# Performance work log

Hardware: AMD Instinct MI355X
Metric: run time of the kernel (lower is better)

Reference implementation:

```python
import jax, jax.numpy as jnp
import numpy as np

S = 192          # spatial_size
N = 100000       # active input sites
CIN, M, M2, NCLS = 3, 32, 64, 50
EPS = 1e-4       # scn BatchNorm eps
OFFS = np.array([[dx, dy, dz] for dx in (-1, 0, 1) for dy in (-1, 0, 1) for dz in (-1, 0, 1)], dtype=np.int64)


def _build_nbr(coords, size):
    # coords: [n,3] unique int64. Returns [n,27] int32 neighbor index (-1 = inactive site),
    # i.e. the submanifold-convolution rulebook built via sorted-key hashing.
    n = coords.shape[0]
    keys = (coords[:, 0] * size + coords[:, 1]) * size + coords[:, 2]
    order = np.argsort(keys)
    sk = keys[order]
    nbr = np.full((n, 27), -1, dtype=np.int32)
    for k, off in enumerate(OFFS):
        nc = coords + off
        ok = np.all((nc >= 0) & (nc < size), axis=1)
        qk = (nc[:, 0] * size + nc[:, 1]) * size + nc[:, 2]
        pos = np.searchsorted(sk, qk).clip(0, n - 1)
        hit = ok & (sk[pos] == qk)
        nbr[hit, k] = order[pos[hit]].astype(np.int32)
    return nbr


def setup_inputs() -> dict:
    rng = np.random.default_rng(0)
    raw = rng.integers(0, S, size=(130000, 3), dtype=np.int64)
    keys = (raw[:, 0] * S + raw[:, 1]) * S + raw[:, 2]
    _, first = np.unique(keys, return_index=True)
    coords = raw[np.sort(first)][:N]          # N unique active voxels
    nbr_fine = _build_nbr(coords, S)
    # stride-2 / filter-2 downsample rulebook: coarse sites = unique(coords // 2)
    S2 = S // 2
    cc = coords // 2
    ckeys = (cc[:, 0] * S2 + cc[:, 1]) * S2 + cc[:, 2]
    uk, parent = np.unique(ckeys, return_inverse=True)
    ccoords = np.column_stack((uk // (S2 * S2), (uk // S2) % S2, uk % S2))
    nbr_coarse = _build_nbr(ccoords, S2)
    offset_id = (coords[:, 0] % 2) * 4 + (coords[:, 1] % 2) * 2 + coords[:, 2] % 2
    key = jax.random.key(0)
    ks = jax.random.split(key, 8)
    def w(k, shape, fan):
        return jax.random.normal(k, shape, jnp.float32) * (1.0 / np.sqrt(fan))
    return dict(
        coords=jnp.asarray(coords, jnp.int32),
        features=jax.random.normal(ks[0], (N, CIN), jnp.float32),
        nbr_fine=jnp.asarray(nbr_fine),
        nbr_coarse=jnp.asarray(nbr_coarse),
        parent=jnp.asarray(parent.astype(np.int32)),
        offset_id=jnp.asarray(offset_id.astype(np.int32)),
        num_coarse=int(uk.shape[0]),
        w_in=w(ks[1], (27, CIN, M), 27 * CIN),
        w_b1=w(ks[2], (27, M, M), 27 * M),
        w_down=w(ks[3], (8, M, M2), 8 * M),
        w_b2=w(ks[4], (27, M2, M2), 27 * M2),
        w_up=w(ks[5], (8, M2, M), 8 * M2),
        w_b3=w(ks[6], (27, 2 * M, M), 27 * 2 * M),
        g1=jnp.ones((M,)), b1=jnp.zeros((M,)),
        gd=jnp.ones((M,)), bd=jnp.zeros((M,)),
        g2=jnp.ones((M2,)), b2=jnp.zeros((M2,)),
        gu=jnp.ones((M2,)), bu=jnp.zeros((M2,)),
        g3=jnp.ones((2 * M,)), b3=jnp.zeros((2 * M,)),
        go=jnp.ones((M,)), bo=jnp.zeros((M,)),
        w_lin=w(ks[7], (M, NCLS), M),
        b_lin=jnp.zeros((NCLS,)),
    )


def _subm_conv(f, nbr, W):
    # f: [n,Cin], nbr: [n,27] (-1 = inactive), W: [27,Cin,Cout]
    mask = nbr >= 0
    g = f[jnp.where(mask, nbr, 0)] * mask[..., None]  # [n,27,Cin]
    return jnp.einsum('nkc,kcd->nd', g, W)


def _bnrelu(f, gamma, beta):
    mu = f.mean(0)
    var = ((f - mu) ** 2).mean(0)
    return jax.nn.relu((f - mu) * (gamma / jnp.sqrt(var + EPS)) + beta)


def _down(f, parent, off_id, W, nc):
    # strided 2^3 conv: out[parent] += W[offset(child)] @ f[child]
    out = jnp.zeros((nc, W.shape[2]), f.dtype)
    for o in range(8):
        sel = (off_id == o)[:, None].astype(f.dtype)
        out = out + jax.ops.segment_sum((f * sel) @ W[o], parent, num_segments=nc)
    return out


def _up(g, parent, off_id, W):
    # 2^3 deconv back to fine sites
    gp = g[parent]
    out = jnp.zeros((gp.shape[0], W.shape[2]), g.dtype)
    for o in range(8):
        out = out + (off_id == o)[:, None].astype(g.dtype) * (gp @ W[o])
    return out


def reference(coords, features, nbr_fine, nbr_coarse, parent, offset_id, num_coarse,
              w_in, w_b1, w_down, w_b2, w_up, w_b3,
              g1, b1, gd, bd, g2, b2, gu, bu, g3, b3, go, bo, w_lin, b_lin):
    # InputLayer (coords unique -> identity) + SubmanifoldConvolution(CIN->M)
    f = _subm_conv(features, nbr_fine, w_in)
    # UNet level 0 block (pre-activation)
    f = _subm_conv(_bnrelu(f, g1, b1), nbr_fine, w_b1)
    skip = f
    # downsample: BNReLU + Convolution(M->M2, 2, 2)
    g = _down(_bnrelu(f, gd, bd), parent, offset_id, w_down, num_coarse)
    # UNet level 1 block
    g = _subm_conv(_bnrelu(g, g2, b2), nbr_coarse, w_b2)
    # upsample: BNReLU + Deconvolution(M2->M, 2, 2)
    u = _up(_bnrelu(g, gu, bu), parent, offset_id, w_up)
    # JoinTable + block (2M -> M)
    f = jnp.concatenate([skip, u], axis=1)
    f = _subm_conv(_bnrelu(f, g3, b3), nbr_fine, w_b3)
    # top-level BatchNormReLU(M) + OutputLayer + Linear head
    f = _bnrelu(f, go, bo)
    return f @ w_lin + b_lin
```

## Files before the change

kernel.cpp:

```cpp
#include <hip/hip_runtime.h>

#define EPS_BN 1e-4f
constexpr int BLK = 256;
constexpr int ECAPC = 1856;
constexpr int NCOPY = 8;

__global__ __launch_bounds__(64) void build_fine_k(
    const int* __restrict__ nbr, int n, int* __restrict__ cnt, int* __restrict__ ent) {
  int i = blockIdx.x * 64 + threadIdx.x;
  if (i >= n) return;
  int c = 0;
  const int* nr = nbr + (size_t)i * 27;
  int* er = ent + (size_t)i * 27;
#pragma unroll 1
  for (int k = 0; k < 27; ++k) {
    int j = nr[k];
    if (j >= 0) er[c++] = (k << 18) | j;
  }
  cnt[i] = c;
}

__global__ __launch_bounds__(64) void build_subm4_k(
    const int* __restrict__ nbr, int n,
    int* __restrict__ segP, int* __restrict__ ent) {
  int T = blockIdx.x, r = threadIdx.x;
  int i = T * 64 + r;
  bool valid = i < n;
  int base = 0;
#pragma unroll 1
  for (int k = 0; k < 27; ++k) {
    int j = valid ? nbr[(size_t)i * 27 + k] : -1;
    bool act = j >= 0;
    unsigned long long mb = __ballot(act);
    int cnt = __popcll(mb);
    int pre = __popcll(mb & ((1ull << r) - 1));
    if (act) ent[(size_t)T * ECAPC + base + pre] = (r << 23) | (k << 18) | j;
    int padded = (cnt + 3) & ~3;
    if (r < padded - cnt) ent[(size_t)T * ECAPC + base + cnt + r] = -1;
    base += padded;
  }
  if (r == 0) segP[T] = base;
}

__global__ __launch_bounds__(BLK) void child_scatter_k(
    const int* __restrict__ parent, const int* __restrict__ offid, int n,
    int* __restrict__ ccnt, int* __restrict__ cent) {
  int i = blockIdx.x * BLK + threadIdx.x;
  if (i >= n) return;
  int p = parent[i];
  int slot = atomicAdd(&ccnt[p], 1);
  cent[p * 8 + slot] = i | (offid[i] << 25);
}

template <int CI, int CO, int MODE>
__global__ __launch_bounds__(BLK) void tconvA_k(
    const float* __restrict__ in, const int* __restrict__ ent, const int* __restrict__ cnt,
    const int* __restrict__ parent, const int* __restrict__ offid,
    const float* __restrict__ W, float* __restrict__ out, int n,
    float* __restrict__ osums) {
  constexpr int LANES = CO / 4, SLOTS = BLK / LANES, RPS = 64 / SLOTS;
  __shared__ float red[2 * CO];
  int t = threadIdx.x;
  for (int idx = t; idx < 2 * CO; idx += BLK) red[idx] = 0.f;
  __syncthreads();
  int slot = t / LANES, lane = t % LANES, g = lane * 4;
  int T = blockIdx.x;
  float ssum[4] = {0, 0, 0, 0}, ssq[4] = {0, 0, 0, 0};
#pragma unroll 1
  for (int rr = 0; rr < RPS; ++rr) {
    int row = T * 64 + slot * RPS + rr;
    bool vrow = row < n;
    float a0 = 0.f, a1 = 0.f, a2 = 0.f, a3 = 0.f;
    int ec = 0;
    if (vrow) ec = (MODE == 2) ? 1 : cnt[row];
#pragma unroll 1
    for (int e = 0; e < ec; ++e) {
      int k, j;
      if constexpr (MODE == 0) {
        int v = ent[(size_t)row * 27 + e];
        k = (v >> 18) & 31; j = v & 0x3FFFF;
      } else if constexpr (MODE == 1) {
        int v = ent[(size_t)row * 8 + e];
        k = v >> 25; j = v & 0x1FFFFFF;
      } else {
        k = offid[row]; j = parent[row];
      }
      const float* Wk = W + (size_t)k * (CI * CO) + g;
      const float* xr = in + (size_t)j * CI;
#pragma unroll
      for (int h = 0; h < CI / 32; ++h) {
        float4 xv[8];
#pragma unroll
        for (int c4 = 0; c4 < 8; ++c4)
          xv[c4] = *reinterpret_cast<const float4*>(xr + h * 32 + c4 * 4);
#pragma unroll
        for (int c4 = 0; c4 < 8; ++c4) {
          float xs[4] = {xv[c4].x, xv[c4].y, xv[c4].z, xv[c4].w};
#pragma unroll
          for (int q = 0; q < 4; ++q) {
            float4 wv = *reinterpret_cast<const float4*>(Wk + (size_t)(h * 32 + c4 * 4 + q) * CO);
            a0 = fmaf(xs[q], wv.x, a0);
            a1 = fmaf(xs[q], wv.y, a1);
            a2 = fmaf(xs[q], wv.z, a2);
            a3 = fmaf(xs[q], wv.w, a3);
          }
        }
      }
    }
    if (vrow)
      *reinterpret_cast<float4*>(out + (size_t)row * CO + g) = make_float4(a0, a1, a2, a3);
    ssum[0] += a0; ssum[1] += a1; ssum[2] += a2; ssum[3] += a3;
    ssq[0] = fmaf(a0, a0, ssq[0]); ssq[1] = fmaf(a1, a1, ssq[1]);
    ssq[2] = fmaf(a2, a2, ssq[2]); ssq[3] = fmaf(a3, a3, ssq[3]);
  }
#pragma unroll
  for (int q = 0; q < 4; ++q) {
    atomicAdd(&red[g + q], ssum[q]);
    atomicAdd(&red[CO + g + q], ssq[q]);
  }
  __syncthreads();
  int copy = blockIdx.x & (NCOPY - 1);
  if (t < 2 * CO) atomicAdd(&osums[copy * 2 * CO + t], red[t]);
}

template <int CI, int CO>
__global__ __launch_bounds__(BLK) void tconvB_k(
    const float* __restrict__ in, const int* __restrict__ segP,
    const int* __restrict__ ent, int ecap,
    const float* __restrict__ W, float* __restrict__ out, int n,
    float* __restrict__ osums) {
  constexpr int GO = CO / 16;
  constexpr int AP = CO + 4;
  __shared__ float lacc[64 * AP];
  int t = threadIdx.x, T = blockIdx.x;
  for (int idx = t; idx < 64 * AP; idx += BLK) lacc[idx] = 0.f;
  __syncthreads();
  int P = segP[T];
  const int* entT = ent + (size_t)T * ecap;
  int slot = t >> 4, g = (t & 15) * GO;
#pragma unroll 1
  for (int pb = slot * 4; pb < P; pb += 64) {
    int ee[4] = {entT[pb], entT[pb + 1], entT[pb + 2], entT[pb + 3]};
    int k = (ee[0] >> 18) & 31;
    const float* Wk = W + (size_t)k * (CI * CO);
    float acc[4][GO];
#pragma unroll
    for (int pp = 0; pp < 4; ++pp)
#pragma unroll
      for (int b = 0; b < GO; ++b) acc[pp][b] = 0.f;
#pragma unroll 4
    for (int c4 = 0; c4 < CI / 4; ++c4) {
      int cb = c4 * 4;
      float xs[4][4];
#pragma unroll
      for (int pp = 0; pp < 4; ++pp) {
        float4 x = make_float4(0.f, 0.f, 0.f, 0.f);
        if (ee[pp] >= 0) {
          int j = ee[pp] & 0x3FFFF;
          x = *reinterpret_cast<const float4*>(in + (size_t)j * CI + cb);
        }
        xs[pp][0] = x.x; xs[pp][1] = x.y; xs[pp][2] = x.z; xs[pp][3] = x.w;
      }
#pragma unroll
      for (int q = 0; q < 4; ++q) {
        float4 w4 = *reinterpret_cast<const float4*>(Wk + (size_t)(cb + q) * CO + g);
        float wv[4] = {w4.x, w4.y, w4.z, w4.w};
#pragma unroll
        for (int pp = 0; pp < 4; ++pp)
#pragma unroll
          for (int b = 0; b < GO; ++b)
            acc[pp][b] = fmaf(xs[pp][q], wv[b], acc[pp][b]);
      }
    }
#pragma unroll
    for (int pp = 0; pp < 4; ++pp) {
      if (ee[pp] >= 0) {
        int r = (ee[pp] >> 23) & 63;
        float* ap = &lacc[r * AP + g];
#pragma unroll
        for (int b = 0; b < GO; ++b) atomicAdd(ap + b, acc[pp][b]);
      }
    }
  }
  __syncthreads();
  for (int idx = t; idx < 64 * (CO / 4); idx += BLK) {
    int r = idx / (CO / 4), c4 = idx - r * (CO / 4);
    int row = T * 64 + r;
    if (row < n)
      *reinterpret_cast<float4*>(out + (size_t)row * CO + c4 * 4) =
          *reinterpret_cast<const float4*>(&lacc[r * AP + c4 * 4]);
  }
  int copy = blockIdx.x & (NCOPY - 1);
  if (t < CO) {
    float s = 0.f, ss = 0.f;
#pragma unroll 4
    for (int r = 0; r < 64; ++r) {
      float x = lacc[r * AP + t];
      s += x; ss = fmaf(x, x, ss);
    }
    atomicAdd(&osums[copy * 2 * CO + t], s);
    atomicAdd(&osums[copy * 2 * CO + CO + t], ss);
  }
}

template <int C>
__global__ __launch_bounds__(BLK) void bnact_k(
    const float* __restrict__ in, const float* __restrict__ sums,
    const float* __restrict__ gm, const float* __restrict__ bt, float invn,
    float* __restrict__ outp, int n) {
  __shared__ float lst[2 * C];
  int t = threadIdx.x;
  if (t < C) {
    float s = 0.f, q = 0.f;
#pragma unroll
    for (int cp = 0; cp < NCOPY; ++cp) { s += sums[cp * 2 * C + t]; q += sums[cp * 2 * C + C + t]; }
    float mu = s * invn, var = q * invn - mu * mu;
    float sc = gm[t] / sqrtf(var + EPS_BN);
    lst[t] = sc; lst[C + t] = bt[t] - mu * sc;
  }
  __syncthreads();
  int total = n * (C / 4);
  const float4* in4 = reinterpret_cast<const float4*>(in);
  float4* out4 = reinterpret_cast<float4*>(outp);
  for (int idx = blockIdx.x * BLK + t; idx < total; idx += gridDim.x * BLK) {
    int cb = (idx & (C / 4 - 1)) * 4;
    float4 x = in4[idx];
    float v[4] = {x.x, x.y, x.z, x.w};
#pragma unroll
    for (int q = 0; q < 4; ++q) {
      float y = fmaf(v[q], lst[cb + q], lst[C + cb + q]);
      v[q] = y > 0.f ? y : 0.f;
    }
    out4[idx] = make_float4(v[0], v[1], v[2], v[3]);
  }
}

__global__ __launch_bounds__(BLK) void bncat_k(
    const float* __restrict__ fa, const float* __restrict__ sA,
    const float* __restrict__ gA, const float* __restrict__ bA,
    const float* __restrict__ fb, const float* __restrict__ sB,
    const float* __restrict__ gB, const float* __restrict__ bB,
    float invn, float* __restrict__ acat, int n) {
  __shared__ float lst[128];
  int t = threadIdx.x;
  if (t < 64) {
    int half = t >> 5, c = t & 31;
    const float* ss = half ? sB : sA;
    const float* gg = half ? gB : gA;
    const float* bb = half ? bB : bA;
    float s = 0.f, q = 0.f;
#pragma unroll
    for (int cp = 0; cp < NCOPY; ++cp) { s += ss[cp * 64 + c]; q += ss[cp * 64 + 32 + c]; }
    float mu = s * invn, var = q * invn - mu * mu;
    float sc = gg[c] / sqrtf(var + EPS_BN);
    lst[half * 64 + c] = sc; lst[half * 64 + 32 + c] = bb[c] - mu * sc;
  }
  __syncthreads();
  int total = n * 16;
  for (int idx = blockIdx.x * BLK + t; idx < total; idx += gridDim.x * BLK) {
    int row = idx >> 4, c4 = idx & 15;
    int half = c4 >> 3, cc = (c4 & 7) * 4;
    const float* src = half ? fb : fa;
    float4 x = *reinterpret_cast<const float4*>(src + (size_t)row * 32 + cc);
    const float* L = lst + half * 64;
    float v[4] = {x.x, x.y, x.z, x.w};
#pragma unroll
    for (int q = 0; q < 4; ++q) {
      float y = fmaf(v[q], L[cc + q], L[32 + cc + q]);
      v[q] = y > 0.f ? y : 0.f;
    }
    *reinterpret_cast<float4*>(acat + (size_t)row * 64 + c4 * 4) = make_float4(v[0], v[1], v[2], v[3]);
  }
}

__global__ __launch_bounds__(BLK) void conv_in_k(
    const float* __restrict__ feat, const int* __restrict__ nbr,
    const float* __restrict__ W, float* __restrict__ out, int n,
    float* __restrict__ osums) {
  int i = blockIdx.x * BLK + threadIdx.x;
  bool valid = i < n;
  float acc[32];
#pragma unroll
  for (int c = 0; c < 32; ++c) acc[c] = 0.f;
#pragma unroll 1
  for (int k = 0; k < 27; ++k) {
    int j = valid ? nbr[(size_t)i * 27 + k] : -1;
    if (j < 0) continue;
    float x0 = feat[j * 3 + 0], x1 = feat[j * 3 + 1], x2 = feat[j * 3 + 2];
    const float* w0 = W + k * 96;
#pragma unroll
    for (int co = 0; co < 8; ++co) {
      float4 a = *reinterpret_cast<const float4*>(w0 + co * 4);
      float4 b = *reinterpret_cast<const float4*>(w0 + 32 + co * 4);
      float4 cc = *reinterpret_cast<const float4*>(w0 + 64 + co * 4);
      acc[4*co+0] = fmaf(x0, a.x, fmaf(x1, b.x, fmaf(x2, cc.x, acc[4*co+0])));
      acc[4*co+1] = fmaf(x0, a.y, fmaf(x1, b.y, fmaf(x2, cc.y, acc[4*co+1])));
      acc[4*co+2] = fmaf(x0, a.z, fmaf(x1, b.z, fmaf(x2, cc.z, acc[4*co+2])));
      acc[4*co+3] = fmaf(x0, a.w, fmaf(x1, b.w, fmaf(x2, cc.w, acc[4*co+3])));
    }
  }
  if (valid) {
    float* o = out + (size_t)i * 32;
#pragma unroll
    for (int co = 0; co < 8; ++co)
      *reinterpret_cast<float4*>(o + co * 4) = make_float4(acc[4*co], acc[4*co+1], acc[4*co+2], acc[4*co+3]);
  }
  __shared__ float red[2][4][32];
  int w = threadIdx.x >> 6;
#pragma unroll
  for (int c = 0; c < 32; ++c) {
    float v = acc[c], q = acc[c] * acc[c];
#pragma unroll
    for (int off = 32; off; off >>= 1) {
      v += __shfl_down(v, off);
      q += __shfl_down(q, off);
    }
    if ((threadIdx.x & 63) == 0) { red[0][w][c] = v; red[1][w][c] = q; }
  }
  __syncthreads();
  if (threadIdx.x < 64) {
    int kind = threadIdx.x >> 5, c = threadIdx.x & 31;
    float s = red[kind][0][c] + red[kind][1][c] + red[kind][2][c] + red[kind][3][c];
    atomicAdd(&osums[(blockIdx.x & (NCOPY - 1)) * 64 + kind * 32 + c], s);
  }
}

__global__ __launch_bounds__(BLK) void head_k(
    const float* __restrict__ fin, const float* __restrict__ sums,
    const float* __restrict__ gm, const float* __restrict__ bt, float inv_n,
    const float* __restrict__ Wl, const float* __restrict__ bl,
    float* __restrict__ out, int n) {
  __shared__ float lw[32 * 50];
  __shared__ float lb[52];
  __shared__ float lst[64];
  int t = threadIdx.x;
  if (t < 32) {
    float s = 0.f, q = 0.f;
#pragma unroll
    for (int cp = 0; cp < NCOPY; ++cp) { s += sums[cp * 64 + t]; q += sums[cp * 64 + 32 + t]; }
    float mu = s * inv_n, var = q * inv_n - mu * mu;
    float sc = gm[t] / sqrtf(var + EPS_BN);
    lst[t] = sc; lst[32 + t] = bt[t] - mu * sc;
  }
  for (int idx = t; idx < 1600; idx += BLK) lw[idx] = Wl[idx];
  if (t < 50) lb[t] = bl[t];
  __syncthreads();
  int i = blockIdx.x * BLK + t;
  if (i >= n) return;
  float x[32];
  const float* fj = fin + (size_t)i * 32;
#pragma unroll
  for (int c4 = 0; c4 < 8; ++c4) {
    float4 v = *reinterpret_cast<const float4*>(fj + c4 * 4);
    float vs[4] = {v.x, v.y, v.z, v.w};
#pragma unroll
    for (int q = 0; q < 4; ++q) {
      int c = c4 * 4 + q;
      float y = fmaf(vs[q], lst[c], lst[32 + c]);
      x[c] = y > 0.f ? y : 0.f;
    }
  }
  float acc[50];
#pragma unroll
  for (int co = 0; co < 50; ++co) acc[co] = lb[co];
#pragma unroll 4
  for (int c = 0; c < 32; ++c) {
#pragma unroll
    for (int co = 0; co < 50; ++co) acc[co] = fmaf(x[c], lw[c * 50 + co], acc[co]);
  }
  float* o = out + (size_t)i * 50;
#pragma unroll
  for (int co = 0; co < 25; ++co)
    *reinterpret_cast<float2*>(o + co * 2) = make_float2(acc[co * 2], acc[co * 2 + 1]);
}

extern "C" void kernel_launch(void* const* d_in, const int* in_sizes, int n_in,
                              void* d_out, int out_size, void* d_ws, size_t ws_size,
                              hipStream_t stream) {
  const float* feat   = (const float*)d_in[1];
  const int*   nbrF   = (const int*)d_in[2];
  const int*   nbrC   = (const int*)d_in[3];
  const int*   parent = (const int*)d_in[4];
  const int*   offid  = (const int*)d_in[5];
  const float* w_in   = (const float*)d_in[7];
  const float* w_b1   = (const float*)d_in[8];
  const float* w_down = (const float*)d_in[9];
  const float* w_b2   = (const float*)d_in[10];
  const float* w_up   = (const float*)d_in[11];
  const float* w_b3   = (const float*)d_in[12];
  const float* g1v = (const float*)d_in[13], *b1v = (const float*)d_in[14];
  const float* gdv = (const float*)d_in[15], *bdv = (const float*)d_in[16];
  const float* g2v = (const float*)d_in[17], *b2v = (const float*)d_in[18];
  const float* guv = (const float*)d_in[19], *buv = (const float*)d_in[20];
  const float* g3v = (const float*)d_in[21], *b3v = (const float*)d_in[22];
  const float* gov = (const float*)d_in[23], *bov = (const float*)d_in[24];
  const float* w_lin = (const float*)d_in[25];
  const float* b_lin = (const float*)d_in[26];
  float* out = (float*)d_out;

  int N  = in_sizes[4];
  int NC = in_sizes[3] / 27;
  int ntF = (N + 63) / 64, ntC = (NC + 63) / 64;

  size_t szF = (size_t)N * 32;
  size_t szG = (size_t)NC * 64;
  size_t SB  = (size_t)N * 64;

  float* ws = (float*)d_ws;
  float* S1 = ws;
  float* S2 = S1 + SB;
  float* S3 = S2 + SB;
  float* S4 = S3 + szF;
  float* S5 = S4 + szF;
  float* sums1 = S5 + szG;
  float* sumsD = sums1 + 8 * 64;
  float* sums2 = sumsD + 8 * 64;
  float* sumsU = sums2 + 8 * 128;
  float* sums4 = sumsU + 8 * 128;
  float* sums5 = sums4 + 8 * 64;
  int* ccnt = (int*)(sums5 + 8 * 64);
  int* cent = ccnt + NC;
  int* cntF = cent + (size_t)NC * 8;
  int* entF = cntF + N;
  int* segPC = entF + (size_t)N * 27;
  int* entC  = segPC + ntC;

  hipMemsetAsync(sums1, 0, (4096 + NC) * sizeof(float), stream);

  int gridN = (N + BLK - 1) / BLK;
  int agrid = 1024;
  float invN = 1.f / (float)N, invC = 1.f / (float)NC;

  build_fine_k<<<ntF, 64, 0, stream>>>(nbrF, N, cntF, entF);
  build_subm4_k<<<ntC, 64, 0, stream>>>(nbrC, NC, segPC, entC);
  child_scatter_k<<<gridN, BLK, 0, stream>>>(parent, offid, N, ccnt, cent);

  conv_in_k<<<gridN, BLK, 0, stream>>>(feat, nbrF, w_in, S1, N, sums1);
  bnact_k<32><<<agrid, BLK, 0, stream>>>(S1, sums1, g1v, b1v, invN, S2, N);

  tconvA_k<32, 32, 0><<<ntF, BLK, 0, stream>>>(
      S2, entF, cntF, nullptr, nullptr, w_b1, S3, N, sumsD);
  bnact_k<32><<<agrid, BLK, 0, stream>>>(S3, sumsD, gdv, bdv, invN, S4, N);

  tconvA_k<32, 64, 1><<<ntC, BLK, 0, stream>>>(
      S4, cent, ccnt, nullptr, nullptr, w_down, S5, NC, sums2);
  bnact_k<64><<<agrid, BLK, 0, stream>>>(S5, sums2, g2v, b2v, invC, S2, NC);

  tconvB_k<64, 64><<<ntC, BLK, 0, stream>>>(
      S2, segPC, entC, ECAPC, w_b2, S1, NC, sumsU);
  bnact_k<64><<<agrid, BLK, 0, stream>>>(S1, sumsU, guv, buv, invC, S5, NC);

  tconvA_k<64, 32, 2><<<ntF, BLK, 0, stream>>>(
      S5, nullptr, nullptr, parent, offid, w_up, S4, N, sums4);

  bncat_k<<<agrid, BLK, 0, stream>>>(
      S3, sumsD, g3v, b3v, S4, sums4, g3v + 32, b3v + 32, invN, S2, N);

  tconvA_k<64, 32, 0><<<ntF, BLK, 0, stream>>>(
      S2, entF, cntF, nullptr, nullptr, w_b3, S3, N, sums5);

  head_k<<<gridN, BLK, 0, stream>>>(S3, sums5, gov, bov, invN, w_lin, b_lin, out, N);
}
```

Before: 586.6 us.

## Restructure coarse submanifold conv as per-offset grouped GEMM with bf16 partials gather

Replaces the per-tile coarse 64->64 submanifold conv with a two-phase scheme. Neighbor pairs are bucketed by kernel offset, and each 128-pair block runs a dense GEMM against that offset's weights held in shared memory, with the BN+ReLU of the input folded into the gather. A separate kernel then sums the per-row partials, which are stored as bf16, and accumulates the BN statistics. This trades the shared-memory atomics and repeated global weight reads for extra bucketing kernels, a partials buffer in memory, and bf16 rounding of the partial products.

```diff
diff --git a/kernel.cpp b/kernel.cpp
--- a/kernel.cpp
+++ b/kernel.cpp
@@ -2,7 +2,6 @@
 
 #define EPS_BN 1e-4f
 constexpr int BLK = 256;
-constexpr int ECAPC = 1856;
 constexpr int NCOPY = 8;
 
 __global__ __launch_bounds__(64) void build_fine_k(
@@ -18,28 +17,6 @@
     if (j >= 0) er[c++] = (k << 18) | j;
   }
   cnt[i] = c;
-}
-
-__global__ __launch_bounds__(64) void build_subm4_k(
-    const int* __restrict__ nbr, int n,
-    int* __restrict__ segP, int* __restrict__ ent) {
-  int T = blockIdx.x, r = threadIdx.x;
-  int i = T * 64 + r;
-  bool valid = i < n;
-  int base = 0;
-#pragma unroll 1
-  for (int k = 0; k < 27; ++k) {
-    int j = valid ? nbr[(size_t)i * 27 + k] : -1;
-    bool act = j >= 0;
-    unsigned long long mb = __ballot(act);
-    int cnt = __popcll(mb);
-    int pre = __popcll(mb & ((1ull << r) - 1));
-    if (act) ent[(size_t)T * ECAPC + base + pre] = (r << 23) | (k << 18) | j;
-    int padded = (cnt + 3) & ~3;
-    if (r < padded - cnt) ent[(size_t)T * ECAPC + base + cnt + r] = -1;
-    base += padded;
-  }
-  if (r == 0) segP[T] = base;
 }
 
 __global__ __launch_bounds__(BLK) void child_scatter_k(
@@ -50,6 +27,178 @@
   int p = parent[i];
   int slot = atomicAdd(&ccnt[p], 1);
   cent[p * 8 + slot] = i | (offid[i] << 25);
+}
+
+__global__ __launch_bounds__(BLK) void kcount_k(
+    const int* __restrict__ nbr, int n, int* __restrict__ kcnt) {
+  __shared__ int lc[27];
+  int t = threadIdx.x;
+  if (t < 27) lc[t] = 0;
+  __syncthreads();
+  int i = blockIdx.x * BLK + t;
+  if (i < n) {
+#pragma unroll 1
+    for (int k = 0; k < 27; ++k)
+      if (nbr[(size_t)i * 27 + k] >= 0) atomicAdd(&lc[k], 1);
+  }
+  __syncthreads();
+  if (t < 27 && lc[t]) atomicAdd(&kcnt[t], lc[t]);
+}
+
+__global__ void kprefix_k(const int* __restrict__ kcnt,
+                          int* __restrict__ segSt, int* __restrict__ kfill) {
+  if (threadIdx.x == 0) {
+    int s = 0;
+#pragma unroll 1
+    for (int k = 0; k < 27; ++k) {
+      segSt[k] = s; kfill[k] = s;
+      s += (kcnt[k] + 127) & ~127;
+    }
+    segSt[27] = s;
+  }
+}
+
+__global__ __launch_bounds__(BLK) void kscatter_k(
+    const int* __restrict__ nbr, int n, int* __restrict__ kfill,
+    int* __restrict__ entJ, int* __restrict__ cntC, int* __restrict__ posC) {
+  int i = blockIdx.x * BLK + threadIdx.x;
+  if (i >= n) return;
+  int c = 0;
+#pragma unroll 1
+  for (int k = 0; k < 27; ++k) {
+    int j = nbr[(size_t)i * 27 + k];
+    if (j >= 0) {
+      int pos = atomicAdd(&kfill[k], 1);
+      entJ[pos] = j;
+      posC[(size_t)i * 27 + c] = pos;
+      ++c;
+    }
+  }
+  cntC[i] = c;
+}
+
+__device__ __forceinline__ unsigned f2bf(float x) {
+  unsigned u = __float_as_uint(x);
+  return (u + 0x7FFFu + ((u >> 16) & 1u)) >> 16;
+}
+
+__global__ __launch_bounds__(128) void pgemm_k(
+    const float* __restrict__ in, const int* __restrict__ segSt,
+    const int* __restrict__ entJ,
+    const float* __restrict__ sums, const float* __restrict__ gm,
+    const float* __restrict__ bt, float invn,
+    const float* __restrict__ W, unsigned short* __restrict__ partials) {
+  __shared__ float lw[4096];
+  __shared__ float lx[128 * 68];
+  __shared__ float lst[128];
+  int t = threadIdx.x;
+  int base = blockIdx.x * 128;
+  if (base >= segSt[27]) return;
+  int k = 0;
+#pragma unroll 1
+  while (segSt[k + 1] <= base) ++k;
+  if (t < 64) {
+    float s = 0.f, q = 0.f;
+#pragma unroll
+    for (int cp = 0; cp < NCOPY; ++cp) { s += sums[cp * 128 + t]; q += sums[cp * 128 + 64 + t]; }
+    float mu = s * invn, var = q * invn - mu * mu;
+    float sc = gm[t] / sqrtf(var + EPS_BN);
+    lst[t] = sc; lst[64 + t] = bt[t] - mu * sc;
+  }
+  const float4* wsrc = reinterpret_cast<const float4*>(W + (size_t)k * 4096);
+#pragma unroll
+  for (int q = 0; q < 8; ++q)
+    reinterpret_cast<float4*>(lw)[t + q * 128] = wsrc[t + q * 128];
+  __syncthreads();
+#pragma unroll 1
+  for (int it = 0; it < 16; ++it) {
+    int idx = t + it * 128;
+    int pr = idx >> 4, cq = idx & 15;
+    int j = entJ[base + pr];
+    float4 x = *reinterpret_cast<const float4*>(in + (size_t)j * 64 + cq * 4);
+    int cb = cq * 4;
+    float y0 = fmaf(x.x, lst[cb + 0], lst[64 + cb + 0]);
+    float y1 = fmaf(x.y, lst[cb + 1], lst[64 + cb + 1]);
+    float y2 = fmaf(x.z, lst[cb + 2], lst[64 + cb + 2]);
+    float y3 = fmaf(x.w, lst[cb + 3], lst[64 + cb + 3]);
+    *reinterpret_cast<float4*>(&lx[pr * 68 + cb]) =
+        make_float4(y0 > 0.f ? y0 : 0.f, y1 > 0.f ? y1 : 0.f,
+                    y2 > 0.f ? y2 : 0.f, y3 > 0.f ? y3 : 0.f);
+  }
+  __syncthreads();
+  int slot = t >> 3, g = (t & 7) * 8;
+  float acc[8][8];
+#pragma unroll
+  for (int pp = 0; pp < 8; ++pp)
+#pragma unroll
+    for (int b = 0; b < 8; ++b) acc[pp][b] = 0.f;
+#pragma unroll
+  for (int c4 = 0; c4 < 16; ++c4) {
+    int cb = c4 * 4;
+    float4 xq[8];
+#pragma unroll
+    for (int pp = 0; pp < 8; ++pp)
+      xq[pp] = *reinterpret_cast<const float4*>(&lx[(slot + 16 * pp) * 68 + cb]);
+#pragma unroll
+    for (int q = 0; q < 4; ++q) {
+      float4 wa = *reinterpret_cast<const float4*>(&lw[(cb + q) * 64 + g]);
+      float4 wb = *reinterpret_cast<const float4*>(&lw[(cb + q) * 64 + g + 4]);
+      float ws[8] = {wa.x, wa.y, wa.z, wa.w, wb.x, wb.y, wb.z, wb.w};
+#pragma unroll
+      for (int pp = 0; pp < 8; ++pp) {
+        float xv = q == 0 ? xq[pp].x : (q == 1 ? xq[pp].y : (q == 2 ? xq[pp].z : xq[pp].w));
+#pragma unroll
+        for (int b = 0; b < 8; ++b) acc[pp][b] = fmaf(xv, ws[b], acc[pp][b]);
+      }
+    }
+  }
+#pragma unroll
+  for (int pp = 0; pp < 8; ++pp) {
+    int p = base + slot + 16 * pp;
+    uint4 o;
+    o.x = f2bf(acc[pp][0]) | (f2bf(acc[pp][1]) << 16);
+    o.y = f2bf(acc[pp][2]) | (f2bf(acc[pp][3]) << 16);
+    o.z = f2bf(acc[pp][4]) | (f2bf(acc[pp][5]) << 16);
+    o.w = f2bf(acc[pp][6]) | (f2bf(acc[pp][7]) << 16);
+    *reinterpret_cast<uint4*>(partials + ((size_t)p * 64 + g)) = o;
+  }
+}
+
+__global__ __launch_bounds__(BLK) void pgather_k(
+    const unsigned short* __restrict__ partials, const int* __restrict__ cntC,
+    const int* __restrict__ posC, float* __restrict__ out, int nc,
+    float* __restrict__ osums) {
+  __shared__ float red[256];
+  int t = threadIdx.x;
+  for (int idx = t; idx < 256; idx += BLK) red[idx] = 0.f;
+  __syncthreads();
+  int slot = t >> 4, g = (t & 15) * 4;
+  int row = blockIdx.x * 16 + slot;
+  float a0 = 0.f, a1 = 0.f, a2 = 0.f, a3 = 0.f;
+  if (row < nc) {
+    int c = cntC[row];
+    const int* pr = posC + (size_t)row * 27;
+#pragma unroll 1
+    for (int e = 0; e < c; ++e) {
+      int pos = pr[e];
+      uint2 u = *reinterpret_cast<const uint2*>(partials + ((size_t)pos * 64 + g));
+      a0 += __uint_as_float(u.x << 16);
+      a1 += __uint_as_float(u.x & 0xFFFF0000u);
+      a2 += __uint_as_float(u.y << 16);
+      a3 += __uint_as_float(u.y & 0xFFFF0000u);
+    }
+    *reinterpret_cast<float4*>(out + (size_t)row * 64 + g) = make_float4(a0, a1, a2, a3);
+  }
+  atomicAdd(&red[g + 0], a0); atomicAdd(&red[g + 1], a1);
+  atomicAdd(&red[g + 2], a2); atomicAdd(&red[g + 3], a3);
+  atomicAdd(&red[128 + g + 0], a0 * a0); atomicAdd(&red[128 + g + 1], a1 * a1);
+  atomicAdd(&red[128 + g + 2], a2 * a2); atomicAdd(&red[128 + g + 3], a3 * a3);
+  __syncthreads();
+  int copy = blockIdx.x & (NCOPY - 1);
+  if (t < 128) {
+    int half = t >> 6, ch = t & 63;
+    atomicAdd(&osums[copy * 128 + half * 64 + ch], red[half * 128 + ch]);
+  }
 }
 
 template <int CI, int CO, int MODE>
@@ -121,86 +270,6 @@
   __syncthreads();
   int copy = blockIdx.x & (NCOPY - 1);
   if (t < 2 * CO) atomicAdd(&osums[copy * 2 * CO + t], red[t]);
-}
-
-template <int CI, int CO>
-__global__ __launch_bounds__(BLK) void tconvB_k(
-    const float* __restrict__ in, const int* __restrict__ segP,
-    const int* __restrict__ ent, int ecap,
-    const float* __restrict__ W, float* __restrict__ out, int n,
-    float* __restrict__ osums) {
-  constexpr int GO = CO / 16;
-  constexpr int AP = CO + 4;
-  __shared__ float lacc[64 * AP];
-  int t = threadIdx.x, T = blockIdx.x;
-  for (int idx = t; idx < 64 * AP; idx += BLK) lacc[idx] = 0.f;
-  __syncthreads();
-  int P = segP[T];
-  const int* entT = ent + (size_t)T * ecap;
-  int slot = t >> 4, g = (t & 15) * GO;
-#pragma unroll 1
-  for (int pb = slot * 4; pb < P; pb += 64) {
-    int ee[4] = {entT[pb], entT[pb + 1], entT[pb + 2], entT[pb + 3]};
-    int k = (ee[0] >> 18) & 31;
-    const float* Wk = W + (size_t)k * (CI * CO);
-    float acc[4][GO];
-#pragma unroll
-    for (int pp = 0; pp < 4; ++pp)
-#pragma unroll
-      for (int b = 0; b < GO; ++b) acc[pp][b] = 0.f;
-#pragma unroll 4
-    for (int c4 = 0; c4 < CI / 4; ++c4) {
-      int cb = c4 * 4;
-      float xs[4][4];
-#pragma unroll
-      for (int pp = 0; pp < 4; ++pp) {
-        float4 x = make_float4(0.f, 0.f, 0.f, 0.f);
-        if (ee[pp] >= 0) {
-          int j = ee[pp] & 0x3FFFF;
-          x = *reinterpret_cast<const float4*>(in + (size_t)j * CI + cb);
-        }
-        xs[pp][0] = x.x; xs[pp][1] = x.y; xs[pp][2] = x.z; xs[pp][3] = x.w;
-      }
-#pragma unroll
-      for (int q = 0; q < 4; ++q) {
-        float4 w4 = *reinterpret_cast<const float4*>(Wk + (size_t)(cb + q) * CO + g);
-        float wv[4] = {w4.x, w4.y, w4.z, w4.w};
-#pragma unroll
-        for (int pp = 0; pp < 4; ++pp)
-#pragma unroll
-          for (int b = 0; b < GO; ++b)
-            acc[pp][b] = fmaf(xs[pp][q], wv[b], acc[pp][b]);
-      }
-    }
-#pragma unroll
-    for (int pp = 0; pp < 4; ++pp) {
-      if (ee[pp] >= 0) {
-        int r = (ee[pp] >> 23) & 63;
-        float* ap = &lacc[r * AP + g];
-#pragma unroll
-        for (int b = 0; b < GO; ++b) atomicAdd(ap + b, acc[pp][b]);
-      }
-    }
-  }
-  __syncthreads();
-  for (int idx = t; idx < 64 * (CO / 4); idx += BLK) {
-    int r = idx / (CO / 4), c4 = idx - r * (CO / 4);
-    int row = T * 64 + r;
-    if (row < n)
-      *reinterpret_cast<float4*>(out + (size_t)row * CO + c4 * 4) =
-          *reinterpret_cast<const float4*>(&lacc[r * AP + c4 * 4]);
-  }
-  int copy = blockIdx.x & (NCOPY - 1);
-  if (t < CO) {
-    float s = 0.f, ss = 0.f;
-#pragma unroll 4
-    for (int r = 0; r < 64; ++r) {
-      float x = lacc[r * AP + t];
-      s += x; ss = fmaf(x, x, ss);
-    }
-    atomicAdd(&osums[copy * 2 * CO + t], s);
-    atomicAdd(&osums[copy * 2 * CO + CO + t], ss);
-  }
 }
 
 template <int C>
@@ -401,6 +470,7 @@
   int N  = in_sizes[4];
   int NC = in_sizes[3] / 27;
   int ntF = (N + 63) / 64, ntC = (NC + 63) / 64;
+  int CAPP = ((NC * 9 / 2) / 128 + 28) * 128;
 
   size_t szF = (size_t)N * 32;
   size_t szG = (size_t)NC * 64;
@@ -422,18 +492,29 @@
   int* cent = ccnt + NC;
   int* cntF = cent + (size_t)NC * 8;
   int* entF = cntF + N;
-  int* segPC = entF + (size_t)N * 27;
-  int* entC  = segPC + ntC;
+  int* kcnt = entF + (size_t)N * 27;
+  int* segSt = kcnt + 32;
+  int* kfill = segSt + 32;
+  int* cntC = kfill + 32;
+  int* posC = cntC + NC;
+  int* entJ = posC + (size_t)NC * 27;
+  unsigned short* partials = (unsigned short*)
+      (((uintptr_t)(entJ + CAPP) + 15) & ~(uintptr_t)15);
 
   hipMemsetAsync(sums1, 0, (4096 + NC) * sizeof(float), stream);
+  hipMemsetAsync(kcnt, 0, 96 * sizeof(int), stream);
+  hipMemsetAsync(entJ, 0, (size_t)CAPP * sizeof(int), stream);
 
   int gridN = (N + BLK - 1) / BLK;
+  int gridC = (NC + BLK - 1) / BLK;
   int agrid = 1024;
   float invN = 1.f / (float)N, invC = 1.f / (float)NC;
 
   build_fine_k<<<ntF, 64, 0, stream>>>(nbrF, N, cntF, entF);
-  build_subm4_k<<<ntC, 64, 0, stream>>>(nbrC, NC, segPC, entC);
   child_scatter_k<<<gridN, BLK, 0, stream>>>(parent, offid, N, ccnt, cent);
+  kcount_k<<<gridC, BLK, 0, stream>>>(nbrC, NC, kcnt);
+  kprefix_k<<<1, 32, 0, stream>>>(kcnt, segSt, kfill);
+  kscatter_k<<<gridC, BLK, 0, stream>>>(nbrC, NC, kfill, entJ, cntC, posC);
 
   conv_in_k<<<gridN, BLK, 0, stream>>>(feat, nbrF, w_in, S1, N, sums1);
   bnact_k<32><<<agrid, BLK, 0, stream>>>(S1, sums1, g1v, b1v, invN, S2, N);
@@ -444,10 +525,13 @@
 
   tconvA_k<32, 64, 1><<<ntC, BLK, 0, stream>>>(
       S4, cent, ccnt, nullptr, nullptr, w_down, S5, NC, sums2);
-  bnact_k<64><<<agrid, BLK, 0, stream>>>(S5, sums2, g2v, b2v, invC, S2, NC);
-
-  tconvB_k<64, 64><<<ntC, BLK, 0, stream>>>(
-      S2, segPC, entC, ECAPC, w_b2, S1, NC, sumsU);
+
+  int gridP1 = CAPP / 128;
+  pgemm_k<<<gridP1, 128, 0, stream>>>(
+      S5, segSt, entJ, sums2, g2v, b2v, invC, w_b2, partials);
+  pgather_k<<<(NC + 15) / 16, BLK, 0, stream>>>(
+      partials, cntC, posC, S1, NC, sumsU);
+
   bnact_k<64><<<agrid, BLK, 0, stream>>>(S1, sumsU, guv, buv, invC, S5, NC);
 
   tconvA_k<64, 32, 2><<<ntF, BLK, 0, stream>>>(
```

Result: slower. 895.3 us (+52.6%).
